# Performance work log

Hardware: AMD Instinct MI355X
Metric: run time of the kernel (lower is better)

Reference implementation:

```python
import jax, jax.numpy as jnp
from jax import lax
import numpy as np

B, C_IN, H, W = 4, 64, 192, 192
NPT = 128          # num_point
MAXC = 32          # objects per image
INIT_STRIDE, COARSE_STRIDE, DOWN = 10.0, 4.0, 4.0


def setup_inputs() -> dict:
    key = jax.random.key(0)
    ks = jax.random.split(key, 8)
    wh_pred = jax.random.normal(ks[0], (B, 2 * NPT, H, W), jnp.float32)
    cnn_feature = jax.random.normal(ks[1], (B, C_IN, H, W), jnp.float32)
    conv1_w = jax.random.normal(ks[2], (256, C_IN, 3, 3), jnp.float32) * 0.05
    conv1_b = jnp.zeros((256,), jnp.float32)
    conv2_w = jax.random.normal(ks[3], (C_IN, 256, 1, 1), jnp.float32) * 0.05
    conv2_b = jnp.zeros((C_IN,), jnp.float32)
    w_poly = jax.random.normal(ks[4], (NPT * 4, (NPT + 1) * C_IN), jnp.float32) * 0.02
    w_fuse = jax.random.normal(ks[5], (NPT * 2, NPT * 4), jnp.float32) * 0.02
    b_fuse = jnp.zeros((NPT * 2,), jnp.float32)
    ct_ind = jax.random.randint(ks[6], (B, MAXC), 0, H * W, jnp.int32)
    ct_img_idx = jnp.repeat(jnp.arange(B, dtype=jnp.int32), MAXC).reshape(B, MAXC)
    ct_num = jnp.full((B,), MAXC, jnp.int32)
    return {"wh_pred": wh_pred, "cnn_feature": cnn_feature,
            "conv1_w": conv1_w, "conv1_b": conv1_b, "conv2_w": conv2_w, "conv2_b": conv2_b,
            "w_poly": w_poly, "w_fuse": w_fuse, "b_fuse": b_fuse,
            "ct_ind": ct_ind, "ct_img_idx": ct_img_idx, "ct_num": ct_num}


def _conv(x, w, b, pad):
    y = lax.conv_general_dilated(x, w, (1, 1), [(pad, pad), (pad, pad)],
                                 dimension_numbers=("NCHW", "OIHW", "NCHW"))
    return y + b[None, :, None, None]


def _pnp(polys, h, w):
    # even-odd ray-casting rasterization: polys [N,P,2] (x,y) -> masks [N,h,w]
    N, P, _ = polys.shape
    yy = jnp.arange(h, dtype=polys.dtype)[None, :, None]   # [1,h,1]
    xx = jnp.arange(w, dtype=polys.dtype)[None, None, :]   # [1,1,w]
    v2 = jnp.roll(polys, -1, axis=1)
    edges = (polys[:, :, 0].T, polys[:, :, 1].T, v2[:, :, 0].T, v2[:, :, 1].T)  # each [P,N]

    def step(par, e):
        x1, y1, x2, y2 = [a[:, None, None] for a in e]      # [N,1,1]
        cond = (y1 > yy) != (y2 > yy)
        den = y2 - y1
        den = jnp.where(jnp.abs(den) < 1e-9, 1e-9, den)
        xint = x1 + (x2 - x1) * (yy - y1) / den
        return jnp.logical_xor(par, cond & (xx < xint)), None

    par0 = jnp.zeros((N, h, w), dtype=bool)
    par, _ = lax.scan(step, par0, edges)
    return par.astype(polys.dtype)


def _mask_batch(mask, ct_num, bs, h, w):
    # faithful to original buggy scatter: offset uses ct_num[i-1], not a cumulative sum
    cn = [int(v) for v in np.asarray(ct_num)]
    mc = max(cn)
    mb = jnp.zeros((bs, mc, h, w), mask.dtype)
    mb = mb.at[0, :cn[0]].set(mask[:cn[0]])
    for i in range(1, bs):
        mb = mb.at[i, :cn[i]].set(mask[cn[i - 1]:cn[i - 1] + cn[i]])
    return mb


def _sample(feat, pts, img_idx):
    # bilinear grid_sample (align_corners=False, zero padding): feat [B,C,H,W], pts [N,P,2] pixel coords
    Bf, C, Hf, Wf = feat.shape
    x = pts[..., 0] - 0.5
    y = pts[..., 1] - 0.5
    x0f = jnp.floor(x); y0f = jnp.floor(y)
    wx = (x - x0f)[..., None]; wy = (y - y0f)[..., None]
    x0 = x0f.astype(jnp.int32); y0 = y0f.astype(jnp.int32)

    def g(xi, yi):
        valid = (xi >= 0) & (xi < Wf) & (yi >= 0) & (yi < Hf)
        v = feat[img_idx[:, None], :, jnp.clip(yi, 0, Hf - 1), jnp.clip(xi, 0, Wf - 1)]  # [N,P,C]
        return v * valid[..., None]

    out = (g(x0, y0) * (1 - wx) * (1 - wy) + g(x0 + 1, y0) * wx * (1 - wy)
           + g(x0, y0 + 1) * (1 - wx) * wy + g(x0 + 1, y0 + 1) * wx * wy)
    return jnp.transpose(out, (0, 2, 1))  # [N,C,P]


def _decode(wh_pred, cnn_feature, conv1_w, conv1_b, conv2_w, conv2_b,
            w_poly, w_fuse, b_fuse, ct_ind, ct_img_idx, ct_num):
    bs, _, h, w = cnn_feature.shape
    ind = ct_ind.reshape(-1)        # ct_01 assumed all valid
    img = ct_img_idx.reshape(-1)
    cx = ind % w
    cy = ind // w
    off = wh_pred[img, :, cy, cx].reshape(ind.shape[0], -1, 2)   # [N, num_point, 2]
    ct = jnp.stack([cx, cy], axis=1).astype(wh_pred.dtype)       # [N,2]
    init_polys = off * INIT_STRIDE + ct[:, None, :]

    # Refine_wtih_pnp.trans_feature
    t = jax.nn.relu(_conv(cnn_feature, conv1_w, conv1_b, 1))
    feat = _conv(t, conv2_w, conv2_b, 0)

    # PnP_contour_feature (init)
    m_init = _pnp(init_polys, h, w)
    mb_init = _mask_batch(m_init, ct_num, bs, h, w)
    feat = jax.nn.relu(jnp.max(mb_init, axis=1, keepdims=True) * feat + feat)

    # GCN-style point feature sampling + global deform
    pts = jnp.concatenate([ct[:, None, :], init_polys], axis=1)  # [N, P+1, 2]
    fp = _sample(feat, pts, img).reshape(ind.shape[0], -1)       # [N, C*(P+1)]
    offsets = ((fp @ w_poly.T) @ w_fuse.T + b_fuse).reshape(-1, NPT, 2)
    coarse = offsets * COARSE_STRIDE + lax.stop_gradient(init_polys)

    # coarse_pnp
    m_c = _pnp(coarse, h, w)
    mb_c = _mask_batch(m_c, ct_num, bs, h, w)
    feat = jax.nn.relu(jnp.max(mb_c, axis=1, keepdims=True) * feat + feat)

    return init_polys * DOWN, coarse * DOWN, mb_init, mb_c, feat


def reference(wh_pred, cnn_feature, conv1_w, conv1_b, conv2_w, conv2_b,
              w_poly, w_fuse, b_fuse, ct_ind, ct_img_idx, ct_num):
    return _decode(wh_pred, cnn_feature, conv1_w, conv1_b, conv2_w, conv2_b,
                   w_poly, w_fuse, b_fuse, ct_ind, ct_img_idx, ct_num)
```

## Files before the change

kernel.cpp:

```cpp
#include <hip/hip_runtime.h>
#include <hip/hip_bf16.h>

#define HH 192
#define WW 192
#define HW 36864
#define CHW 2359296

typedef __attribute__((ext_vector_type(8))) short short8;
typedef __attribute__((ext_vector_type(4))) float float4v;
typedef __attribute__((ext_vector_type(4))) unsigned short ushort4v;

static __device__ __forceinline__ unsigned short f2bu(float f) {
  union { float f; unsigned u; } v; v.f = f;
  unsigned r = (v.u + 0x7fffu + ((v.u >> 16) & 1u)) >> 16;
  return (unsigned short)r;
}

static __device__ __forceinline__ float bu2f(unsigned short s) {
  union { unsigned u; float f; } v; v.u = ((unsigned)s) << 16;
  return v.f;
}

__global__ void k_prep(const float* __restrict__ c1w, const float* __restrict__ c2w,
                       const float* __restrict__ wfuse,
                       unsigned short* __restrict__ wB1, unsigned short* __restrict__ wB2,
                       float* __restrict__ wfT,
                       const float* __restrict__ wh, const int* __restrict__ ct_ind,
                       const int* __restrict__ ct_img,
                       float* __restrict__ initp, float* __restrict__ out0) {
  int blk = blockIdx.x;
  if (blk >= 1152) {
    int n = blk - 1152;
    int p = threadIdx.x;
    if (p < 128) {
      int ind = ct_ind[n], img = ct_img[n];
      int cx = ind % WW, cy = ind / WW;
      size_t base = ((size_t)(img * 256 + 2 * p)) * HW + (size_t)cy * WW + cx;
      float ox = wh[base];
      float oy = wh[base + HW];
      float px = __fadd_rn(__fmul_rn(ox, 10.0f), (float)cx);
      float py = __fadd_rn(__fmul_rn(oy, 10.0f), (float)cy);
      initp[n * 256 + 2 * p]     = px;
      initp[n * 256 + 2 * p + 1] = py;
      out0[n * 256 + 2 * p]      = __fmul_rn(px, 4.0f);
      out0[n * 256 + 2 * p + 1]  = __fmul_rn(py, 4.0f);
    }
    return;
  }
  int i = blk * 256 + threadIdx.x;
  if (i < 147456) {
    int T = i / 9216, r = i % 9216;
    int s = r / 512, e = r % 512;
    int l = e >> 3, j = e & 7;
    int m = l & 15, q = l >> 4;
    int oc = T * 16 + m;
    int k = s * 32 + q * 8 + j;
    int tap = k >> 6, ic = k & 63;
    int ky = tap / 3, kx = tap % 3;
    wB1[i] = f2bu(c1w[((oc * 64 + ic) * 3 + ky) * 3 + kx]);
    return;
  }
  int j2 = i - 147456;
  if (j2 < 16384) {
    int g = j2 / 512, e = j2 % 512;
    int l = e >> 3, jj = e & 7;
    int m = l & 15, q = l >> 4;
    int w = g / 8, s2 = g % 8;
    wB2[j2] = f2bu(c2w[(w * 16 + m) * 256 + s2 * 32 + q * 8 + jj]);
    return;
  }
  int k3 = j2 - 16384;
  if (k3 < 131072) { int jj = k3 >> 8, r = k3 & 255; wfT[k3] = wfuse[r * 512 + jj]; }
}

__global__ __launch_bounds__(256) void k_pnp(const float* __restrict__ polys,
    float* __restrict__ outm, float* __restrict__ uout,
    float* __restrict__ fgate, const unsigned short* __restrict__ fsrc) {
  int row = blockIdx.x;
  int b   = blockIdx.y;
  int t = threadIdx.x;
  int w = t >> 6, lane = t & 63;
  __shared__ __align__(16) char smem[40960];
  float (*xint)[128] = (float (*)[128])smem;
  float (*mrow)[192] = (float (*)[192])(smem + 16384);
  unsigned short* frow = (unsigned short*)smem;
  __shared__ int   cnt[32];
  __shared__ float urow[192];
  if (t < 32) cnt[t] = 0;
  __syncthreads();
  int nbase = (b == 0) ? 0 : 32;
  float yy = (float)row;
  for (int pc = 0; pc < 8; ++pc) {
    int c = w * 8 + pc;
    const float* P = polys + (nbase + c) * 256;
    for (int e = lane; e < 128; e += 64) {
      float y1 = P[2 * e + 1], y2 = P[2 * ((e + 1) & 127) + 1];
      if ((y1 > yy) != (y2 > yy)) {
        float x1 = P[2 * e], x2 = P[2 * ((e + 1) & 127)];
        float den = __fsub_rn(y2, y1);
        if (fabsf(den) < 1e-9f) den = 1e-9f;
        float xi = __fadd_rn(x1, __fdiv_rn(__fmul_rn(__fsub_rn(x2, x1), __fsub_rn(yy, y1)), den));
        xint[c][atomicAdd(&cnt[c], 1)] = xi;
      }
    }
  }
  __syncthreads();
  for (int idx = t; idx < 32 * 192; idx += 256) {
    int c = idx / 192, xp = idx - c * 192;
    float xf = (float)xp;
    int mm = cnt[c], cr = 0;
    for (int j = 0; j < mm; ++j) cr += (xf < xint[c][j]) ? 1 : 0;
    float mv = (float)(cr & 1);
    mrow[c][xp] = mv;
    outm[((size_t)(b * 32 + c) * HH + row) * WW + xp] = mv;
  }
  __syncthreads();
  if (t < 192) {
    float u = 0.f;
#pragma unroll
    for (int c = 0; c < 32; ++c) u = fmaxf(u, mrow[c][t]);
    urow[t] = u;
    if (uout) uout[(size_t)b * HW + (size_t)row * WW + t] = u;
  }
  __syncthreads();
  if (fgate) {
    const unsigned short* fr = fsrc + ((size_t)b * HW + (size_t)row * WW) * 64;
    for (int idx = t; idx < 3072; idx += 256)
      ((ushort4v*)frow)[idx] = ((const ushort4v*)fr)[idx];
    __syncthreads();
    float* fb = fgate + (size_t)b * CHW + (size_t)row * WW;
    for (int idx = t; idx < 3072; idx += 256) {
      int chn = idx / 48, qx = idx - chn * 48;
      float4v o;
#pragma unroll
      for (int j = 0; j < 4; ++j) {
        int xp = qx * 4 + j;
        float f = bu2f(frow[xp * 64 + chn]);
        float uu = urow[xp];
        o[j] = fmaxf(__fadd_rn(__fmul_rn(uu, f), f), 0.f);
      }
      *(float4v*)&fb[(size_t)chn * HW + qx * 4] = o;
    }
  }
}

__global__ __launch_bounds__(256, 3) void k_conv(const float* __restrict__ x,
    const unsigned short* __restrict__ wB1, const float* __restrict__ b1,
    const unsigned short* __restrict__ wB2, const float* __restrict__ b2,
    const float* __restrict__ u0, unsigned short* __restrict__ featT) {
  int blk = blockIdx.x;
  int b    = blk / 576;
  int rem  = blk % 576;
  int pair = rem / 6;
  int xs   = rem % 6;
  int y0 = pair * 2, x0 = xs * 32;
  int t = threadIdx.x;
  int w = t >> 6, l = t & 63;
  int m = l & 15, q = l >> 4;

  __shared__ __align__(16) unsigned short sb[16896];

  {
    int kq = t & 7;
    int pr = t >> 3;
    for (int itr = 0; itr < 8; ++itr) {
      int pi = itr * 32 + pr;
      int r  = pi >> 6;
      int ic = pi & 63;
      int gy = y0 + r - 1;
      float4v v = (float4v){0.f, 0.f, 0.f, 0.f};
      if (gy >= 0 && gy < HH)
        v = *(const float4v*)&x[(size_t)(b * 64 + ic) * HW + (size_t)gy * WW + x0 + kq * 4];
      int base = (r * 34 + 1 + kq * 4) * 72 + ic;
      sb[base]       = f2bu(v[0]);
      sb[base + 72]  = f2bu(v[1]);
      sb[base + 144] = f2bu(v[2]);
      sb[base + 216] = f2bu(v[3]);
    }
    for (int itr = 0; itr < 2; ++itr) {
      int e = itr * 256 + t;
      int xxh = e >> 8;
      int rm = e & 255;
      int r = rm >> 6, ic = rm & 63;
      int gy = y0 + r - 1;
      int gx = x0 - 1 + xxh * 33;
      float v = 0.f;
      if (gy >= 0 && gy < HH && gx >= 0 && gx < WW)
        v = x[(size_t)(b * 64 + ic) * HW + (size_t)gy * WW + gx];
      sb[(r * 34 + xxh * 33) * 72 + ic] = f2bu(v);
    }
  }
  __syncthreads();

  float4v acc1[4][4];
#pragma unroll
  for (int nt = 0; nt < 4; ++nt) {
    float bv = b1[w * 64 + nt * 16 + m];
#pragma unroll
    for (int mt = 0; mt < 4; ++mt) acc1[mt][nt] = (float4v){bv, bv, bv, bv};
  }

#pragma unroll
  for (int s = 0; s < 18; ++s) {
    int tap = s >> 1, ky = tap / 3, kx = tap - ky * 3;
    int ic0 = (s & 1) * 32 + q * 8;
    short8 bF[4];
#pragma unroll
    for (int nt = 0; nt < 4; ++nt)
      bF[nt] = *(const short8*)&wB1[(size_t)((((w * 4 + nt) * 18 + s) * 512) + l * 8)];
    short8 aF[4];
#pragma unroll
    for (int mt = 0; mt < 4; ++mt) {
      int col  = (mt & 1) * 16 + m + kx;
      int rowi = ky + (mt >> 1);
      aF[mt] = *(const short8*)&sb[(rowi * 34 + col) * 72 + ic0];
    }
#pragma unroll
    for (int nt = 0; nt < 4; ++nt)
#pragma unroll
      for (int mt = 0; mt < 4; ++mt)
        acc1[mt][nt] = __builtin_amdgcn_mfma_f32_16x16x32_bf16(aF[mt], bF[nt], acc1[mt][nt], 0, 0, 0);
  }
  __syncthreads();

#pragma unroll
  for (int mt = 0; mt < 4; ++mt)
#pragma unroll
    for (int nt = 0; nt < 4; ++nt)
#pragma unroll
      for (int r = 0; r < 4; ++r) {
        int p = mt * 16 + q * 4 + r;
        int oc = w * 64 + nt * 16 + m;
        sb[p * 264 + oc] = f2bu(fmaxf(acc1[mt][nt][r], 0.f));
      }
  __syncthreads();

  float4v acc2[4];
  {
    float bv = b2[w * 16 + m];
#pragma unroll
    for (int mt = 0; mt < 4; ++mt) acc2[mt] = (float4v){bv, bv, bv, bv};
  }
#pragma unroll
  for (int s2 = 0; s2 < 8; ++s2) {
    short8 bF2 = *(const short8*)&wB2[(size_t)(((w * 8 + s2) * 512) + l * 8)];
#pragma unroll
    for (int mt = 0; mt < 4; ++mt) {
      short8 a2 = *(const short8*)&sb[(mt * 16 + m) * 264 + s2 * 32 + q * 8];
      acc2[mt] = __builtin_amdgcn_mfma_f32_16x16x32_bf16(a2, bF2, acc2[mt], 0, 0, 0);
    }
  }
  __syncthreads();

  float* fS = (float*)sb;
#pragma unroll
  for (int mt = 0; mt < 4; ++mt)
#pragma unroll
    for (int r = 0; r < 4; ++r) {
      int p = mt * 16 + q * 4 + r;
      fS[w * 1088 + m * 68 + p] = acc2[mt][r];
    }
  const float* ub = u0 + b * HW;
  {
    unsigned short* ft = featT + (size_t)b * HW * 64;
    int c2 = (l & 7) * 2;
#pragma unroll
    for (int i = 0; i < 8; ++i) {
      int p = (l >> 3) + 8 * i;
      float f0 = fS[w * 1088 + c2 * 68 + p];
      float f1 = fS[w * 1088 + (c2 + 1) * 68 + p];
      int gy = y0 + (p >> 5), gx = x0 + (p & 31);
      float uu = ub[gy * WW + gx];
      f0 = fmaxf(uu * f0 + f0, 0.f);
      f1 = fmaxf(uu * f1 + f1, 0.f);
      unsigned v = (unsigned)f2bu(f0) | ((unsigned)f2bu(f1) << 16);
      *(unsigned*)&ft[((size_t)(gy * WW + gx)) * 64 + w * 16 + c2] = v;
    }
  }
}

__global__ __launch_bounds__(256) void k_sample(const unsigned short* __restrict__ featT,
    const float* __restrict__ initp, const int* __restrict__ ct_ind,
    const int* __restrict__ ct_img, float* __restrict__ fp) {
  int n  = blockIdx.x;
  int ch = blockIdx.y;
  int t  = threadIdx.x;
  int w  = t >> 6, lane = t & 63;
  int c  = lane & 31;
  int ph = lane >> 5;

  __shared__ float sF[4128];

  int img = ct_img[n];
  int ind = ct_ind[n];
  float ctx = (float)(ind % WW), cty = (float)(ind / WW);
  const unsigned short* fb = featT + (size_t)img * HW * 64 + ch * 32 + c;

  for (int i = 0; i < 17; ++i) {
    int p = i * 8 + w * 2 + ph;
    if (p < 129) {
      float px, py;
      if (p == 0) { px = ctx; py = cty; }
      else {
        px = initp[n * 256 + 2 * (p - 1)];
        py = initp[n * 256 + 2 * (p - 1) + 1];
      }
      float x = __fsub_rn(px, 0.5f), y = __fsub_rn(py, 0.5f);
      float x0f = floorf(x), y0f = floorf(y);
      float wx = __fsub_rn(x, x0f), wy = __fsub_rn(y, y0f);
      int x0 = (int)x0f, y0 = (int)y0f;
      float g[4];
#pragma unroll
      for (int qq = 0; qq < 4; ++qq) {
        int xi = x0 + (qq & 1), yi = y0 + (qq >> 1);
        bool valid = (xi >= 0) && (xi < WW) && (yi >= 0) && (yi < HH);
        int xc = min(max(xi, 0), WW - 1), yc = min(max(yi, 0), HH - 1);
        float v = bu2f(fb[(size_t)(yc * WW + xc) * 64]);
        g[qq] = valid ? v : 0.f;
      }
      float omx = __fsub_rn(1.f, wx), omy = __fsub_rn(1.f, wy);
      float r = __fadd_rn(__fadd_rn(__fadd_rn(
          __fmul_rn(__fmul_rn(g[0], omx), omy),
          __fmul_rn(__fmul_rn(g[1], wx),  omy)),
          __fmul_rn(__fmul_rn(g[2], omx), wy)),
          __fmul_rn(__fmul_rn(g[3], wx),  wy));
      sF[c * 129 + p] = r;
    }
  }
  __syncthreads();
  float* dst = fp + (size_t)n * 8256 + (size_t)ch * 4128;
  for (int idx = t; idx < 4128; idx += 256) dst[idx] = sF[idx];
}

__global__ __launch_bounds__(256) void k_gemm1(const float* __restrict__ fp,
    const float* __restrict__ wpoly, float* __restrict__ part) {
  int ntile = blockIdx.x;
  int jtile = blockIdx.y;
  int ks    = blockIdx.z;
  int c0 = (129 * ks) / 32, c1 = (129 * (ks + 1)) / 32;
  int t = threadIdx.x;
  int tn = t & 15, tj = t >> 4;
  __shared__ __align__(16) float aS[64][68];
  __shared__ __align__(16) float bS[64][68];
  float acc[4][4];
#pragma unroll
  for (int i = 0; i < 4; ++i)
#pragma unroll
    for (int j = 0; j < 4; ++j) acc[i][j] = 0.f;
  for (int ch = c0; ch < c1; ++ch) {
    int k0 = ch * 64;
    __syncthreads();
    for (int idx = t; idx < 1024; idx += 256) {
      int r = idx >> 4, c4 = (idx & 15) * 4;
      float4v va = *(const float4v*)&fp[(size_t)(ntile * 64 + r) * 8256 + k0 + c4];
      float4v vb = *(const float4v*)&wpoly[(size_t)(jtile * 64 + r) * 8256 + k0 + c4];
#pragma unroll
      for (int d = 0; d < 4; ++d) { aS[c4 + d][r] = va[d]; bS[c4 + d][r] = vb[d]; }
    }
    __syncthreads();
    for (int kk = 0; kk < 64; ++kk) {
      float4v a = *(const float4v*)&aS[kk][tn * 4];
      float4v bq = *(const float4v*)&bS[kk][tj * 4];
      acc[0][0] = fmaf(a[0], bq[0], acc[0][0]); acc[0][1] = fmaf(a[0], bq[1], acc[0][1]);
      acc[0][2] = fmaf(a[0], bq[2], acc[0][2]); acc[0][3] = fmaf(a[0], bq[3], acc[0][3]);
      acc[1][0] = fmaf(a[1], bq[0], acc[1][0]); acc[1][1] = fmaf(a[1], bq[1], acc[1][1]);
      acc[1][2] = fmaf(a[1], bq[2], acc[1][2]); acc[1][3] = fmaf(a[1], bq[3], acc[1][3]);
      acc[2][0] = fmaf(a[2], bq[0], acc[2][0]); acc[2][1] = fmaf(a[2], bq[1], acc[2][1]);
      acc[2][2] = fmaf(a[2], bq[2], acc[2][2]); acc[2][3] = fmaf(a[2], bq[3], acc[2][3]);
      acc[3][0] = fmaf(a[3], bq[0], acc[3][0]); acc[3][1] = fmaf(a[3], bq[1], acc[3][1]);
      acc[3][2] = fmaf(a[3], bq[2], acc[3][2]); acc[3][3] = fmaf(a[3], bq[3], acc[3][3]);
    }
  }
  float* dst = part + (size_t)ks * 65536;
#pragma unroll
  for (int i = 0; i < 4; ++i) {
    float4v o = (float4v){acc[i][0], acc[i][1], acc[i][2], acc[i][3]};
    *(float4v*)&dst[(size_t)(ntile * 64 + tn * 4 + i) * 512 + jtile * 64 + tj * 4] = o;
  }
}

__global__ __launch_bounds__(256) void k_gemm2(const float* __restrict__ part,
    const float* __restrict__ wfT, const float* __restrict__ bfuse,
    const float* __restrict__ initp, float* __restrict__ coarse, float* __restrict__ out1) {
  int n = blockIdx.x, r = threadIdx.x;
  __shared__ float tS[512];
  float s0 = 0.f, s1 = 0.f;
  for (int ks = 0; ks < 32; ++ks) {
    const float* p = part + (size_t)ks * 65536 + (size_t)n * 512;
    s0 = __fadd_rn(s0, p[r]);
    s1 = __fadd_rn(s1, p[r + 256]);
  }
  tS[r] = s0;
  tS[r + 256] = s1;
  __syncthreads();
  float acc = 0.f;
  for (int j = 0; j < 512; ++j) acc = fmaf(wfT[j * 256 + r], tS[j], acc);
  acc = __fadd_rn(acc, bfuse[r]);
  float cr = __fadd_rn(__fmul_rn(acc, 4.0f), initp[n * 256 + r]);
  coarse[n * 256 + r] = cr;
  out1[n * 256 + r] = __fmul_rn(cr, 4.0f);
}

extern "C" void kernel_launch(void* const* d_in, const int* in_sizes, int n_in,
                              void* d_out, int out_size, void* d_ws, size_t ws_size,
                              hipStream_t stream) {
  const float* wh    = (const float*)d_in[0];
  const float* cnnf  = (const float*)d_in[1];
  const float* c1w   = (const float*)d_in[2];
  const float* c1b   = (const float*)d_in[3];
  const float* c2w   = (const float*)d_in[4];
  const float* c2b   = (const float*)d_in[5];
  const float* wpoly = (const float*)d_in[6];
  const float* wfuse = (const float*)d_in[7];
  const float* bfuse = (const float*)d_in[8];
  const int* ct_ind  = (const int*)d_in[9];
  const int* ct_img  = (const int*)d_in[10];

  float* ws    = (float*)d_ws;
  float* wfT   = ws;
  float* initp = wfT + 131072;
  float* coarse= initp + 32768;
  float* u0    = coarse + 32768;
  float* fpbuf = u0 + 147456;
  float* part  = fpbuf + 1056768;
  unsigned short* wB1 = (unsigned short*)(part + 2097152);
  unsigned short* wB2 = wB1 + 147456;
  unsigned short* featT = wB2 + 16384;

  float* out0 = (float*)d_out;
  float* out1 = out0 + 32768;
  float* out2 = out1 + 32768;
  float* out3 = out2 + 4718592;
  float* out4 = out3 + 4718592;

  k_prep<<<1280, 256, 0, stream>>>(c1w, c2w, wfuse, wB1, wB2, wfT,
                                   wh, ct_ind, ct_img, initp, out0);
  k_pnp<<<dim3(192, 4), 256, 0, stream>>>(initp, out2, u0, nullptr, nullptr);
  k_conv<<<2304, 256, 0, stream>>>(cnnf, wB1, c1b, wB2, c2b, u0, featT);
  k_sample<<<dim3(128, 2), 256, 0, stream>>>(featT, initp, ct_ind, ct_img, fpbuf);
  k_gemm1<<<dim3(2, 8, 32), 256, 0, stream>>>(fpbuf, wpoly, part);
  k_gemm2<<<128, 256, 0, stream>>>(part, wfT, bfuse, initp, coarse, out1);
  k_pnp<<<dim3(192, 4), 256, 0, stream>>>(coarse, out3, nullptr, out4, featT);
}
```

Baseline: 413.0 us.

## Split conv block across eight waves to halve per-wave accumulators

Doubles the fused conv kernel's block from 256 to 512 threads, so each wave holds 2 instead of 4 output-channel tiles in the 3x3 conv MFMA stage. The 1x1 conv stage is repartitioned across waves by (row tile, channel pair). The epilogue now stages all 64 channels per pixel in shared memory and writes contiguous per-pixel rows to featT. The aim is lower register pressure and more waves in flight to hide latency, at the cost of an extra barrier and duplicated A-fragment loads across waves.

New measurement: 423.8 us. +2.6%, slower.

```diff
diff --git a/kernel.cpp b/kernel.cpp
--- a/kernel.cpp
+++ b/kernel.cpp
@@ -144,7 +144,7 @@
   }
 }
 
-__global__ __launch_bounds__(256, 3) void k_conv(const float* __restrict__ x,
+__global__ __launch_bounds__(512, 4) void k_conv(const float* __restrict__ x,
     const unsigned short* __restrict__ wB1, const float* __restrict__ b1,
     const unsigned short* __restrict__ wB2, const float* __restrict__ b2,
     const float* __restrict__ u0, unsigned short* __restrict__ featT) {
@@ -163,8 +163,8 @@
   {
     int kq = t & 7;
     int pr = t >> 3;
-    for (int itr = 0; itr < 8; ++itr) {
-      int pi = itr * 32 + pr;
+    for (int itr = 0; itr < 4; ++itr) {
+      int pi = itr * 64 + pr;
       int r  = pi >> 6;
       int ic = pi & 63;
       int gy = y0 + r - 1;
@@ -177,10 +177,9 @@
       sb[base + 144] = f2bu(v[2]);
       sb[base + 216] = f2bu(v[3]);
     }
-    for (int itr = 0; itr < 2; ++itr) {
-      int e = itr * 256 + t;
-      int xxh = e >> 8;
-      int rm = e & 255;
+    {
+      int xxh = t >> 8;
+      int rm = t & 255;
       int r = rm >> 6, ic = rm & 63;
       int gy = y0 + r - 1;
       int gx = x0 - 1 + xxh * 33;
@@ -192,10 +191,10 @@
   }
   __syncthreads();
 
-  float4v acc1[4][4];
-#pragma unroll
-  for (int nt = 0; nt < 4; ++nt) {
-    float bv = b1[w * 64 + nt * 16 + m];
+  float4v acc1[4][2];
+#pragma unroll
+  for (int nt = 0; nt < 2; ++nt) {
+    float bv = b1[(w * 2 + nt) * 16 + m];
 #pragma unroll
     for (int mt = 0; mt < 4; ++mt) acc1[mt][nt] = (float4v){bv, bv, bv, bv};
   }
@@ -204,10 +203,10 @@
   for (int s = 0; s < 18; ++s) {
     int tap = s >> 1, ky = tap / 3, kx = tap - ky * 3;
     int ic0 = (s & 1) * 32 + q * 8;
-    short8 bF[4];
-#pragma unroll
-    for (int nt = 0; nt < 4; ++nt)
-      bF[nt] = *(const short8*)&wB1[(size_t)((((w * 4 + nt) * 18 + s) * 512) + l * 8)];
+    short8 bF[2];
+#pragma unroll
+    for (int nt = 0; nt < 2; ++nt)
+      bF[nt] = *(const short8*)&wB1[(size_t)((((w * 2 + nt) * 18 + s) * 512) + l * 8)];
     short8 aF[4];
 #pragma unroll
     for (int mt = 0; mt < 4; ++mt) {
@@ -216,7 +215,7 @@
       aF[mt] = *(const short8*)&sb[(rowi * 34 + col) * 72 + ic0];
     }
 #pragma unroll
-    for (int nt = 0; nt < 4; ++nt)
+    for (int nt = 0; nt < 2; ++nt)
 #pragma unroll
       for (int mt = 0; mt < 4; ++mt)
         acc1[mt][nt] = __builtin_amdgcn_mfma_f32_16x16x32_bf16(aF[mt], bF[nt], acc1[mt][nt], 0, 0, 0);
@@ -226,56 +225,54 @@
 #pragma unroll
   for (int mt = 0; mt < 4; ++mt)
 #pragma unroll
-    for (int nt = 0; nt < 4; ++nt)
+    for (int nt = 0; nt < 2; ++nt)
 #pragma unroll
       for (int r = 0; r < 4; ++r) {
         int p = mt * 16 + q * 4 + r;
-        int oc = w * 64 + nt * 16 + m;
+        int oc = (w * 2 + nt) * 16 + m;
         sb[p * 264 + oc] = f2bu(fmaxf(acc1[mt][nt][r], 0.f));
       }
   __syncthreads();
 
-  float4v acc2[4];
-  {
-    float bv = b2[w * 16 + m];
-#pragma unroll
-    for (int mt = 0; mt < 4; ++mt) acc2[mt] = (float4v){bv, bv, bv, bv};
+  int mt2 = w >> 1, ntb = (w & 1) * 2;
+  float4v acc2[2];
+#pragma unroll
+  for (int i = 0; i < 2; ++i) {
+    float bv = b2[(ntb + i) * 16 + m];
+    acc2[i] = (float4v){bv, bv, bv, bv};
   }
 #pragma unroll
   for (int s2 = 0; s2 < 8; ++s2) {
-    short8 bF2 = *(const short8*)&wB2[(size_t)(((w * 8 + s2) * 512) + l * 8)];
-#pragma unroll
-    for (int mt = 0; mt < 4; ++mt) {
-      short8 a2 = *(const short8*)&sb[(mt * 16 + m) * 264 + s2 * 32 + q * 8];
-      acc2[mt] = __builtin_amdgcn_mfma_f32_16x16x32_bf16(a2, bF2, acc2[mt], 0, 0, 0);
+    short8 a2 = *(const short8*)&sb[(mt2 * 16 + m) * 264 + s2 * 32 + q * 8];
+#pragma unroll
+    for (int i = 0; i < 2; ++i) {
+      short8 bF2 = *(const short8*)&wB2[(size_t)((((ntb + i) * 8 + s2) * 512) + l * 8)];
+      acc2[i] = __builtin_amdgcn_mfma_f32_16x16x32_bf16(a2, bF2, acc2[i], 0, 0, 0);
     }
   }
   __syncthreads();
 
   float* fS = (float*)sb;
 #pragma unroll
-  for (int mt = 0; mt < 4; ++mt)
-#pragma unroll
-    for (int r = 0; r < 4; ++r) {
-      int p = mt * 16 + q * 4 + r;
-      fS[w * 1088 + m * 68 + p] = acc2[mt][r];
-    }
+  for (int i = 0; i < 2; ++i)
+#pragma unroll
+    for (int r = 0; r < 4; ++r)
+      fS[(mt2 * 16 + q * 4 + r) * 68 + (ntb + i) * 16 + m] = acc2[i][r];
+  __syncthreads();
   const float* ub = u0 + b * HW;
-  {
-    unsigned short* ft = featT + (size_t)b * HW * 64;
-    int c2 = (l & 7) * 2;
-#pragma unroll
-    for (int i = 0; i < 8; ++i) {
-      int p = (l >> 3) + 8 * i;
-      float f0 = fS[w * 1088 + c2 * 68 + p];
-      float f1 = fS[w * 1088 + (c2 + 1) * 68 + p];
-      int gy = y0 + (p >> 5), gx = x0 + (p & 31);
-      float uu = ub[gy * WW + gx];
-      f0 = fmaxf(uu * f0 + f0, 0.f);
-      f1 = fmaxf(uu * f1 + f1, 0.f);
-      unsigned v = (unsigned)f2bu(f0) | ((unsigned)f2bu(f1) << 16);
-      *(unsigned*)&ft[((size_t)(gy * WW + gx)) * 64 + w * 16 + c2] = v;
-    }
+  unsigned short* ft = featT + (size_t)b * HW * 64;
+#pragma unroll
+  for (int i = 0; i < 4; ++i) {
+    int idx = i * 512 + t;
+    int p = idx >> 5, cp = idx & 31;
+    int gy = y0 + (p >> 5), gx = x0 + (p & 31);
+    float uu = ub[gy * WW + gx];
+    float f0 = fS[p * 68 + cp * 2];
+    float f1 = fS[p * 68 + cp * 2 + 1];
+    f0 = fmaxf(uu * f0 + f0, 0.f);
+    f1 = fmaxf(uu * f1 + f1, 0.f);
+    unsigned v = (unsigned)f2bu(f0) | ((unsigned)f2bu(f1) << 16);
+    *(unsigned*)&ft[((size_t)(gy * WW + gx)) * 64 + cp * 2] = v;
   }
 }
 
@@ -436,7 +433,7 @@
   k_prep<<<1280, 256, 0, stream>>>(c1w, c2w, wfuse, wB1, wB2, wfT,
                                    wh, ct_ind, ct_img, initp, out0);
   k_pnp<<<dim3(192, 4), 256, 0, stream>>>(initp, out2, u0, nullptr, nullptr);
-  k_conv<<<2304, 256, 0, stream>>>(cnnf, wB1, c1b, wB2, c2b, u0, featT);
+  k_conv<<<2304, 512, 0, stream>>>(cnnf, wB1, c1b, wB2, c2b, u0, featT);
   k_sample<<<dim3(128, 2), 256, 0, stream>>>(featT, initp, ct_ind, ct_img, fpbuf);
   k_gemm1<<<dim3(2, 8, 32), 256, 0, stream>>>(fpbuf, wpoly, part);
   k_gemm2<<<128, 256, 0, stream>>>(part, wfT, bfuse, initp, coarse, out1);
```
